# Optimization experiments

Hardware: AMD Instinct MI355X
Metric: run time of the kernel (lower is better)

The kernel has to match this reference:

```python
import jax, jax.numpy as jnp
import numpy as np

B, T, D = 4, 2048, 1024
H, DH, E, SEL = 8, 64, 5, 2


def setup_inputs() -> dict:
    key = jax.random.key(0)
    ks = jax.random.split(key, 7)
    s = 0.02
    x = jax.random.normal(ks[0], (B, T, D), dtype=jnp.float32)
    Wq = jax.random.normal(ks[1], (D, H * DH), dtype=jnp.float32) * s
    Wk = jax.random.normal(ks[2], (D, H * DH), dtype=jnp.float32) * s
    Ws = jax.random.normal(ks[3], (D, H * E), dtype=jnp.float32) * s   # gate for V experts
    Wd = jax.random.normal(ks[4], (D, H * E), dtype=jnp.float32) * s   # gate for out experts
    Wv = jax.random.normal(ks[5], (E, D, DH), dtype=jnp.float32) * s   # experts_v weights
    Wo = jax.random.normal(ks[6], (E, DH, D), dtype=jnp.float32) * s   # experts_out weights
    return {"x": x, "Wq": Wq, "Wk": Wk, "Ws": Ws, "Wd": Wd, "Wv": Wv, "Wo": Wo}


def _topk_mask(logits, k):
    # 0/1 mask of top-k experts along last axis (torch.topk indices are distinct)
    _, idx = jax.lax.top_k(logits, k)
    return jnp.sum(jax.nn.one_hot(idx, logits.shape[-1], dtype=logits.dtype), axis=-2)


def reference(x, Wq, Wk, Ws, Wd, Wv, Wo):
    e, d, dh = Wv.shape
    h = Wq.shape[1] // dh
    b, t, _ = x.shape
    scale = dh ** -0.5

    q = (x @ Wq).reshape(b, t, h, dh).transpose(0, 2, 1, 3)  # b h t d
    k = (x @ Wk).reshape(b, t, h, dh).transpose(0, 2, 1, 3)  # b h t d

    # moe_v: per-(b,t,head) top-k experts, sigmoid-weighted combine of expert V projections
    gl_v = (x @ Ws).reshape(b, t, h, e)                      # b t h e
    wv = _topk_mask(gl_v, SEL) * jax.nn.sigmoid(gl_v)        # b t h e (zero off selected)
    xv = jnp.einsum('btd,edk->btek', x, Wv)                  # all-expert V: b t e dh
    v = jnp.einsum('bthe,btek->bhtk', wv, xv)                # b h t dh

    scores = jnp.einsum('bhid,bhjd->bhij', q * scale, k)     # b h t t
    probs = jax.nn.softmax(scores, axis=-1)
    attn = jnp.einsum('bhij,bhjd->bihd', probs, v)           # b t h dh

    # moe_out: top-k selection (weights computed but unused in original), unweighted sum,
    # then sum over heads — fuse both reductions into one einsum
    gl_o = (x @ Wd).reshape(b, t, h, e)
    mask_o = _topk_mask(gl_o, SEL)                           # b t h e
    out = jnp.einsum('bthe,bthk,ekd->btd', mask_o, attn, Wo)  # b t d
    return out
```

## Files before the change

### kernel.cpp

```cpp
#include <hip/hip_runtime.h>
#include <cstdint>
#include <cstddef>

#define BB 4
#define TT 2048
#define DD 1024
#define HH 8
#define DH 64
#define EE 5
#define MM (BB*TT)
#define PLD 1344
#define NWT 1408

typedef short short8 __attribute__((ext_vector_type(8)));
typedef float f32x4  __attribute__((ext_vector_type(4)));
typedef float f32x16 __attribute__((ext_vector_type(16)));
typedef unsigned int u32x2 __attribute__((ext_vector_type(2)));

__device__ __forceinline__ float bflo(uint32_t u) { union { uint32_t i; float f; } v; v.i = u << 16; return v.f; }
__device__ __forceinline__ float bfhi(uint32_t u) { union { uint32_t i; float f; } v; v.i = u & 0xFFFF0000u; return v.f; }
__device__ __forceinline__ float bf2f(uint16_t u) { union { uint32_t i; float f; } v; v.i = ((uint32_t)u) << 16; return v.f; }
__device__ __forceinline__ uint32_t pkbf(float a, float b) {
  uint32_t ua = __float_as_uint(a) + 0x8000u;
  uint32_t ub = __float_as_uint(b) + 0x8000u;
  return __builtin_amdgcn_perm(ub, ua, 0x07060302u);
}
__device__ __forceinline__ uint16_t bfr1(float f) {
  return (uint16_t)((__float_as_uint(f) + 0x8000u) >> 16);
}
__device__ __forceinline__ uint32_t cvtpk(float a, float b) {
  uint32_t r;
  asm("v_cvt_pk_bf16_f32 %0, %1, %2" : "=v"(r) : "v"(a), "v"(b));
  return r;
}

__device__ __forceinline__ void gload16(const void* g, void* l) {
  __builtin_amdgcn_global_load_lds(
      (const __attribute__((address_space(1))) uint32_t*)g,
      (__attribute__((address_space(3))) uint32_t*)l, 16, 0, 0);
}

__global__ __launch_bounds__(256) void pack_wt_kernel(
    const float* __restrict__ Wq, const float* __restrict__ Wk,
    const float* __restrict__ Wv, uint16_t* __restrict__ Wt)
{
  __shared__ __align__(16) uint16_t Ts[64 * 68];
  int k0 = blockIdx.x * 64, n0 = blockIdx.y * 64;
  int t = threadIdx.x;
#pragma unroll
  for (int rep = 0; rep < 16; ++rep) {
    int li = rep * 256 + t;
    int kl = li >> 6, nl = li & 63;
    int k = k0 + kl, n = n0 + nl;
    float v = 0.f;
    if (n < 512)       v = Wq[k * 512 + n];
    else if (n < 1024) v = Wk[k * 512 + (n - 512)];
    else if (n < 1344) { int nn = n - 1024; v = Wv[((size_t)(nn >> 6) * 1024 + k) * 64 + (nn & 63)]; }
    Ts[kl * 68 + nl] = bfr1(v);
  }
  __syncthreads();
#pragma unroll
  for (int rep = 0; rep < 16; ++rep) {
    int li = rep * 256 + t;
    int nl = li >> 6, kl = li & 63;
    Wt[(size_t)(n0 + nl) * 1024 + k0 + kl] = Ts[kl * 68 + nl];
  }
}

__global__ __launch_bounds__(256) void pack_wot_kernel(
    const float* __restrict__ Wo, uint16_t* __restrict__ WoT)
{
  __shared__ __align__(16) uint16_t Ts[64 * 68];
  int k0 = blockIdx.x * 64, n0 = blockIdx.y * 64;
  int t = threadIdx.x;
#pragma unroll
  for (int rep = 0; rep < 16; ++rep) {
    int li = rep * 256 + t;
    int kl = li >> 6, nl = li & 63;
    Ts[kl * 68 + nl] = bfr1(Wo[(size_t)(k0 + kl) * 1024 + n0 + nl]);
  }
  __syncthreads();
#pragma unroll
  for (int rep = 0; rep < 16; ++rep) {
    int li = rep * 256 + t;
    int nl = li >> 6, kl = li & 63;
    WoT[(size_t)(n0 + nl) * 320 + k0 + kl] = Ts[kl * 68 + nl];
  }
}

__global__ __launch_bounds__(256) void xbf_kernel(const float* __restrict__ x, uint16_t* __restrict__ xb)
{
  int i = (blockIdx.x * 256 + threadIdx.x) * 4;
  float4 v = *(const float4*)(x + i);
  uint2 o;
  o.x = pkbf(v.x, v.y);
  o.y = pkbf(v.z, v.w);
  *(uint2*)(xb + i) = o;
}

__device__ __forceinline__ void top2_5(float g0, float g1, float g2, float g3, float g4,
                                       int& i1, float& b1, int& i2, float& b2) {
  i1 = 0; b1 = g0;
  if (g1 > b1) { b1 = g1; i1 = 1; }
  if (g2 > b1) { b1 = g2; i1 = 2; }
  if (g3 > b1) { b1 = g3; i1 = 3; }
  if (g4 > b1) { b1 = g4; i1 = 4; }
  i2 = -1; b2 = -__builtin_inff();
  if (i1 != 0 && g0 > b2) { b2 = g0; i2 = 0; }
  if (i1 != 1 && g1 > b2) { b2 = g1; i2 = 1; }
  if (i1 != 2 && g2 > b2) { b2 = g2; i2 = 2; }
  if (i1 != 3 && g3 > b2) { b2 = g3; i2 = 3; }
  if (i1 != 4 && g4 > b2) { b2 = g4; i2 = 4; }
}

__device__ __forceinline__ void ldw20(float* d, const float* __restrict__ p) {
#pragma unroll
  for (int j = 0; j < 20; ++j) d[j] = p[j];
}
__device__ __forceinline__ void fma20(float* acc, const float* wv, float xv) {
#pragma unroll
  for (int j = 0; j < 20; ++j) acc[j] = fmaf(xv, wv[j], acc[j]);
}

__global__ __launch_bounds__(1024) void gate_v6_kernel(
    const float* __restrict__ x, const float* __restrict__ Ws,
    const float* __restrict__ Wd, uint32_t* __restrict__ gsel32)
{
  __shared__ __align__(16) float xs[10752];
  int t = threadIdx.x;
  int m0 = blockIdx.x * 64;
  int g  = blockIdx.y;
  int w = t >> 6, lane = t & 63;
  int cg = __builtin_amdgcn_readfirstlane(w & 1);
  int kq = __builtin_amdgcn_readfirstlane(w >> 1);
  const float* __restrict__ Wg = g ? Wd : Ws;
  const float* __restrict__ wbase = Wg + (size_t)(kq * 16) * 40 + cg * 20;

  float acc[20];
#pragma unroll
  for (int j = 0; j < 20; ++j) acc[j] = 0.f;

  for (int tile = 0; tile < 8; ++tile) {
    __syncthreads();
#pragma unroll
    for (int rep = 0; rep < 2; ++rep) {
      int li = rep * 1024 + t;
      int row = li >> 5, kg = li & 31;
      float4 v = *(const float4*)&x[(size_t)(m0 + row) * 1024 + tile * 128 + kg * 4];
      *(float4*)&xs[row * 132 + kg * 4] = v;
    }
    __syncthreads();

    const float* wp = wbase + (size_t)tile * 128 * 40;
    const float* xp = &xs[lane * 132 + kq * 16];
    float wc[20], wn[20];
    ldw20(wc, wp);
#pragma unroll
    for (int k4 = 0; k4 < 4; ++k4) {
      float4 xv = *(const float4*)&xp[k4 * 4];
      ldw20(wn, wp + (size_t)(k4 * 4 + 1) * 40);
      fma20(acc, wc, xv.x);
      ldw20(wc, wp + (size_t)(k4 * 4 + 2) * 40);
      fma20(acc, wn, xv.y);
      ldw20(wn, wp + (size_t)(k4 * 4 + 3) * 40);
      fma20(acc, wc, xv.z);
      if (k4 < 3) ldw20(wc, wp + (size_t)(k4 * 4 + 4) * 40);
      fma20(acc, wn, xv.w);
    }
  }

  float* red = xs;
  __syncthreads();
  if (kq & 1) {
    int ro = (((kq >> 1) * 2 + cg) * 64 + lane) * 21;
#pragma unroll
    for (int j = 0; j < 20; ++j) red[ro + j] = acc[j];
  }
  __syncthreads();
  if (!(kq & 1)) {
    int ro = (((kq >> 1) * 2 + cg) * 64 + lane) * 21;
#pragma unroll
    for (int j = 0; j < 20; ++j) acc[j] += red[ro + j];
  }
  __syncthreads();
  if (kq == 2 || kq == 6) {
    int ro = (((kq >> 2) * 2 + cg) * 64 + lane) * 21;
#pragma unroll
    for (int j = 0; j < 20; ++j) red[ro + j] = acc[j];
  }
  __syncthreads();
  if (kq == 0 || kq == 4) {
    int ro = (((kq >> 2) * 2 + cg) * 64 + lane) * 21;
#pragma unroll
    for (int j = 0; j < 20; ++j) acc[j] += red[ro + j];
  }
  __syncthreads();
  if (kq == 4) {
    int ro = (cg * 64 + lane) * 21;
#pragma unroll
    for (int j = 0; j < 20; ++j) red[ro + j] = acc[j];
  }
  __syncthreads();

  if (kq == 0) {
    int ro = (cg * 64 + lane) * 21;
#pragma unroll
    for (int j = 0; j < 20; ++j) acc[j] += red[ro + j];
    int m = m0 + lane;
    if (g == 0) {
#pragma unroll
      for (int hh = 0; hh < 4; ++hh) {
        int i1, i2; float b1, b2;
        top2_5(acc[hh * 5 + 0], acc[hh * 5 + 1], acc[hh * 5 + 2],
               acc[hh * 5 + 3], acc[hh * 5 + 4], i1, b1, i2, b2);
        float w1 = 1.f / (1.f + __expf(-b1));
        float w2 = 1.f / (1.f + __expf(-b2));
        uint32_t* gp = gsel32 + ((size_t)m * 8 + cg * 4 + hh) * 4;
        gp[0] = __float_as_uint(w1);
        gp[1] = __float_as_uint(w2);
        gp[2] = (uint32_t)(i1 | (i2 << 3));
      }
    } else {
#pragma unroll
      for (int hh = 0; hh < 4; ++hh) {
        int j1, j2; float c1, c2;
        top2_5(acc[hh * 5 + 0], acc[hh * 5 + 1], acc[hh * 5 + 2],
               acc[hh * 5 + 3], acc[hh * 5 + 4], j1, c1, j2, c2);
        uint32_t* gp = gsel32 + ((size_t)m * 8 + cg * 4 + hh) * 4;
        gp[3] = (uint32_t)(j1 | (j2 << 3));
      }
    }
  }
}

__global__ __launch_bounds__(256) void proj_mfma_kernel(
    const uint16_t* __restrict__ xb, const uint16_t* __restrict__ Wt,
    uint16_t* __restrict__ proj)
{
  __shared__ __align__(16) uint16_t As[128 * 32];
  __shared__ __align__(16) uint16_t Bs[128 * 32];
  int t = threadIdx.x;
  int n0 = blockIdx.x * 128, m0 = blockIdx.y * 128;
  int w = t >> 6, lane = t & 63, q = lane >> 4, c = lane & 15;
  int wm = w & 1, wn = w >> 1;
  int lr = lane >> 2, lc = (lane & 3) * 8;
  f32x4 zf = {0.f, 0.f, 0.f, 0.f};
  f32x4 acc[4][4];
#pragma unroll
  for (int i = 0; i < 4; ++i)
#pragma unroll
    for (int j = 0; j < 4; ++j) acc[i][j] = zf;

  for (int kb = 0; kb < 32; ++kb) {
    __syncthreads();
#pragma unroll
    for (int j = 0; j < 2; ++j) {
      int row = w * 32 + j * 16 + lr;
      gload16(xb + (size_t)(m0 + row) * 1024 + kb * 32 + lc,
              &As[(w * 32 + j * 16) * 32 + lane * 8]);
      gload16(Wt + (size_t)(n0 + row) * 1024 + kb * 32 + lc,
              &Bs[(w * 32 + j * 16) * 32 + lane * 8]);
    }
    __syncthreads();
    short8 af[4], bfr[4];
#pragma unroll
    for (int i = 0; i < 4; ++i)
      af[i] = *(const short8*)&As[(wm * 64 + i * 16 + c) * 32 + q * 8];
#pragma unroll
    for (int j = 0; j < 4; ++j)
      bfr[j] = *(const short8*)&Bs[(wn * 64 + j * 16 + c) * 32 + q * 8];
#pragma unroll
    for (int i = 0; i < 4; ++i)
#pragma unroll
      for (int j = 0; j < 4; ++j)
        acc[i][j] = __builtin_amdgcn_mfma_f32_16x16x32_bf16(af[i], bfr[j], acc[i][j], 0, 0, 0);
  }
#pragma unroll
  for (int i = 0; i < 4; ++i)
#pragma unroll
    for (int j = 0; j < 4; ++j) {
      int col = n0 + wn * 64 + j * 16 + c;
      if (col < PLD) {
#pragma unroll
        for (int reg = 0; reg < 4; ++reg) {
          int row = m0 + wm * 64 + i * 16 + q * 4 + reg;
          proj[(size_t)row * PLD + col] = bfr1(acc[i][j][reg]);
        }
      }
    }
}

__global__ __launch_bounds__(256) void out_mfma_kernel(
    const uint16_t* __restrict__ zb, const uint16_t* __restrict__ WoT,
    float* __restrict__ out)
{
  __shared__ __align__(16) uint16_t As[128 * 32];
  __shared__ __align__(16) uint16_t Bs[128 * 32];
  int t = threadIdx.x;
  int n0 = blockIdx.x * 128, m0 = blockIdx.y * 128;
  int w = t >> 6, lane = t & 63, q = lane >> 4, c = lane & 15;
  int wm = w & 1, wn = w >> 1;
  int lr = lane >> 2, lc = (lane & 3) * 8;
  f32x4 zf = {0.f, 0.f, 0.f, 0.f};
  f32x4 acc[4][4];
#pragma unroll
  for (int i = 0; i < 4; ++i)
#pragma unroll
    for (int j = 0; j < 4; ++j) acc[i][j] = zf;

  for (int kb = 0; kb < 10; ++kb) {
    __syncthreads();
#pragma unroll
    for (int j = 0; j < 2; ++j) {
      int row = w * 32 + j * 16 + lr;
      gload16(zb + (size_t)(m0 + row) * 320 + kb * 32 + lc,
              &As[(w * 32 + j * 16) * 32 + lane * 8]);
      gload16(WoT + (size_t)(n0 + row) * 320 + kb * 32 + lc,
              &Bs[(w * 32 + j * 16) * 32 + lane * 8]);
    }
    __syncthreads();
    short8 af[4], bfr[4];
#pragma unroll
    for (int i = 0; i < 4; ++i)
      af[i] = *(const short8*)&As[(wm * 64 + i * 16 + c) * 32 + q * 8];
#pragma unroll
    for (int j = 0; j < 4; ++j)
      bfr[j] = *(const short8*)&Bs[(wn * 64 + j * 16 + c) * 32 + q * 8];
#pragma unroll
    for (int i = 0; i < 4; ++i)
#pragma unroll
      for (int j = 0; j < 4; ++j)
        acc[i][j] = __builtin_amdgcn_mfma_f32_16x16x32_bf16(af[i], bfr[j], acc[i][j], 0, 0, 0);
  }
#pragma unroll
  for (int i = 0; i < 4; ++i)
#pragma unroll
    for (int j = 0; j < 4; ++j) {
      int col = n0 + wn * 64 + j * 16 + c;
#pragma unroll
      for (int reg = 0; reg < 4; ++reg) {
        int row = m0 + wm * 64 + i * 16 + q * 4 + reg;
        out[(size_t)row * 1024 + col] = acc[i][j][reg];
      }
    }
}

__global__ __launch_bounds__(256) void vbuild_kernel(
    const uint16_t* __restrict__ proj, const uint4* __restrict__ gsel,
    uint16_t* __restrict__ vt)
{
  int bi = blockIdx.x;
  int bh = bi >> 5, tb = bi & 31;
  int b = bh >> 3, h = bh & 7;
  int t = threadIdx.x;
  int tt = t & 63, dg = t >> 6;
  int m = b * 2048 + tb * 64 + tt;
  uint4 gs = gsel[m * 8 + h];
  float w1 = __uint_as_float(gs.x), w2 = __uint_as_float(gs.y);
  int i1 = gs.z & 7, i2 = (gs.z >> 3) & 7;
  const uint16_t* base = proj + (size_t)m * PLD + 1024;
  const uint4* p1 = (const uint4*)(base + i1 * 64 + dg * 16);
  const uint4* p2 = (const uint4*)(base + i2 * 64 + dg * 16);
  uint4 A0 = p1[0], A1 = p1[1], B0 = p2[0], B1 = p2[1];
  float v[16];
  v[0]  = w1*bflo(A0.x) + w2*bflo(B0.x); v[1]  = w1*bfhi(A0.x) + w2*bfhi(B0.x);
  v[2]  = w1*bflo(A0.y) + w2*bflo(B0.y); v[3]  = w1*bfhi(A0.y) + w2*bfhi(B0.y);
  v[4]  = w1*bflo(A0.z) + w2*bflo(B0.z); v[5]  = w1*bfhi(A0.z) + w2*bfhi(B0.z);
  v[6]  = w1*bflo(A0.w) + w2*bflo(B0.w); v[7]  = w1*bfhi(A0.w) + w2*bfhi(B0.w);
  v[8]  = w1*bflo(A1.x) + w2*bflo(B1.x); v[9]  = w1*bfhi(A1.x) + w2*bfhi(B1.x);
  v[10] = w1*bflo(A1.y) + w2*bflo(B1.y); v[11] = w1*bfhi(A1.y) + w2*bfhi(B1.y);
  v[12] = w1*bflo(A1.z) + w2*bflo(B1.z); v[13] = w1*bfhi(A1.z) + w2*bfhi(B1.z);
  v[14] = w1*bflo(A1.w) + w2*bflo(B1.w); v[15] = w1*bfhi(A1.w) + w2*bfhi(B1.w);
#pragma unroll
  for (int dd = 0; dd < 16; ++dd)
    vt[(size_t)(bh * 64 + dg * 16 + dd) * 2048 + tb * 64 + tt] = bfr1(v[dd]);
}

__global__ __launch_bounds__(512) void flash_mfma_kernel(
    const uint16_t* __restrict__ proj, const uint16_t* __restrict__ vt,
    uint16_t* __restrict__ attnb)
{
  __shared__ __align__(16) char smem[36864];
  int t = threadIdx.x;
  int bx = blockIdx.x;
  int qb = bx & 15, bh = bx >> 4;
  int h = bh & 7, b = bh >> 3;
  int g = t >> 8;
  int tg = t & 255;
  int w = t >> 6, wl = w & 3;
  int lane = t & 63;
  int r31 = lane & 31, hi = lane >> 5;
  int srow = tg >> 2, scq = tg & 3;

  uint16_t* Ksg = (uint16_t*)smem + g * 4608;
  uint16_t* Vsg = (uint16_t*)smem + 9216 + g * 4608;

  short8 qf[4];
  {
    const uint16_t* qp = proj + (size_t)(b * 2048 + qb * 128 + wl * 32 + r31) * PLD + h * 64 + hi * 8;
#pragma unroll
    for (int f = 0; f < 4; ++f) qf[f] = *(const short8*)(qp + 16 * f);
  }

  f32x16 o0 = {0.f}, o1 = {0.f};
#pragma unroll
  for (int i = 0; i < 16; ++i) { o0[i] = 0.f; o1[i] = 0.f; }
  float lsacc = 0.f;

  const uint16_t* kg = proj + (size_t)(b * 2048 + g * 1024 + srow) * PLD + 512 + h * 64 + scq * 16;
  const uint16_t* vg = vt + (size_t)(bh * 64 + srow) * 2048 + g * 1024 + scq * 16;
  uint4 kp0, kp1, vp0, vp1;
  kp0 = ((const uint4*)kg)[0]; kp1 = ((const uint4*)kg)[1];
  vp0 = ((const uint4*)vg)[0]; vp1 = ((const uint4*)vg)[1];

  for (int it = 0; it < 16; ++it) {
    if (it) __syncthreads();
    *(uint4*)&Ksg[srow * 72 + scq * 16] = kp0;
    *(uint4*)&Ksg[srow * 72 + scq * 16 + 8] = kp1;
    *(uint4*)&Vsg[srow * 72 + scq * 16] = vp0;
    *(uint4*)&Vsg[srow * 72 + scq * 16 + 8] = vp1;
    __syncthreads();
    if (it < 15) {
      const uint4* pk = (const uint4*)(kg + (size_t)(it + 1) * 64 * PLD);
      kp0 = pk[0]; kp1 = pk[1];
      const uint4* pv = (const uint4*)(vg + (it + 1) * 64);
      vp0 = pv[0]; vp1 = pv[1];
    }

    short8 pa[4];
#pragma unroll
    for (int jg = 0; jg < 2; ++jg) {
      f32x16 s;
#pragma unroll
      for (int i = 0; i < 16; ++i) s[i] = 0.f;
#pragma unroll
      for (int f = 0; f < 4; ++f) {
        short8 kf = *(const short8*)&Ksg[(jg * 32 + r31) * 72 + hi * 8 + 16 * f];
        s = __builtin_amdgcn_mfma_f32_32x32x16_bf16(kf, qf[f], s, 0, 0, 0);
      }
      float p[16];
#pragma unroll
      for (int reg = 0; reg < 16; ++reg)
        p[reg] = __builtin_amdgcn_exp2f(s[reg] * 0.18033688f);
      lsacc += (((p[0] + p[1]) + (p[2] + p[3])) + ((p[4] + p[5]) + (p[6] + p[7])))
             + (((p[8] + p[9]) + (p[10] + p[11])) + ((p[12] + p[13]) + (p[14] + p[15])));
      uint32_t X1 = cvtpk(p[0], p[1]),  X2 = cvtpk(p[2], p[3]);
      uint32_t Y1 = cvtpk(p[4], p[5]),  Y2 = cvtpk(p[6], p[7]);
      uint32_t Z1 = cvtpk(p[8], p[9]),  Z2 = cvtpk(p[10], p[11]);
      uint32_t W1 = cvtpk(p[12], p[13]), W2 = cvtpk(p[14], p[15]);
      u32x2 s1 = __builtin_amdgcn_permlane32_swap(X1, Y1, false, false);
      u32x2 s2 = __builtin_amdgcn_permlane32_swap(X2, Y2, false, false);
      u32x2 s3 = __builtin_amdgcn_permlane32_swap(Z1, W1, false, false);
      u32x2 s4 = __builtin_amdgcn_permlane32_swap(Z2, W2, false, false);
      uint4 f0 = { s1.x, s2.x, s1.y, s2.y };
      uint4 f1 = { s3.x, s4.x, s3.y, s4.y };
      pa[jg * 2 + 0] = *(short8*)&f0;
      pa[jg * 2 + 1] = *(short8*)&f1;
    }

#pragma unroll
    for (int f = 0; f < 4; ++f) {
      short8 vf0 = *(const short8*)&Vsg[(r31) * 72 + hi * 8 + 16 * f];
      short8 vf1 = *(const short8*)&Vsg[(32 + r31) * 72 + hi * 8 + 16 * f];
      o0 = __builtin_amdgcn_mfma_f32_32x32x16_bf16(pa[f], vf0, o0, 0, 0, 0);
      o1 = __builtin_amdgcn_mfma_f32_32x32x16_bf16(pa[f], vf1, o1, 0, 0, 0);
    }
  }

  float lsc = lsacc + __shfl_xor(lsacc, 32);
  __syncthreads();
  float* xch = (float*)smem;
  float* xls = (float*)(smem + 33792);
  float* lsb = (float*)(smem + 34304);
  if (g == 1) {
    int base = (wl * 64 + lane) * 33;
#pragma unroll
    for (int reg = 0; reg < 16; ++reg) {
      xch[base + reg] = o0[reg];
      xch[base + 16 + reg] = o1[reg];
    }
    if (lane < 32) xls[wl * 32 + r31] = lsc;
  }
  __syncthreads();
  if (g == 0) {
    int base = (wl * 64 + lane) * 33;
#pragma unroll
    for (int reg = 0; reg < 16; ++reg) {
      o0[reg] += xch[base + reg];
      o1[reg] += xch[base + 16 + reg];
    }
    float lst = lsc + xls[wl * 32 + r31];
    if (lane < 32) lsb[wl * 32 + r31] = 1.0f / lst;
#pragma unroll
    for (int reg = 0; reg < 16; ++reg) {
      int r = (reg & 3) + 8 * (reg >> 2) + 4 * hi;
      float inv = lsb[wl * 32 + r];
      size_t row = (size_t)(b * 2048 + qb * 128 + wl * 32 + r);
      attnb[row * 512 + h * 64 + r31]      = bfr1(o0[reg] * inv);
      attnb[row * 512 + h * 64 + 32 + r31] = bfr1(o1[reg] * inv);
    }
  }
}

__global__ __launch_bounds__(64) void zbuild_kernel(
    const uint16_t* __restrict__ attnb, const uint32_t* __restrict__ gselw,
    uint16_t* __restrict__ zbuf)
{
  int m = blockIdx.x; int c = threadIdx.x;
  float acc[5] = {0.f, 0.f, 0.f, 0.f, 0.f};
#pragma unroll
  for (int h = 0; h < 8; ++h) {
    uint32_t sel = gselw[(m * 8 + h) * 4 + 3];
    int e1 = sel & 7, e2 = (sel >> 3) & 7;
    float a = bf2f(attnb[(size_t)m * 512 + h * 64 + c]);
#pragma unroll
    for (int e = 0; e < 5; ++e)
      acc[e] += (e == e1 || e == e2) ? a : 0.f;
  }
#pragma unroll
  for (int e = 0; e < 5; ++e)
    zbuf[(size_t)m * 320 + e * 64 + c] = bfr1(acc[e]);
}

extern "C" void kernel_launch(void* const* d_in, const int* in_sizes, int n_in,
                              void* d_out, int out_size, void* d_ws, size_t ws_size,
                              hipStream_t stream) {
  const float* x  = (const float*)d_in[0];
  const float* Wq = (const float*)d_in[1];
  const float* Wk = (const float*)d_in[2];
  const float* Ws = (const float*)d_in[3];
  const float* Wd = (const float*)d_in[4];
  const float* Wv = (const float*)d_in[5];
  const float* Wo = (const float*)d_in[6];
  float* out = (float*)d_out;

  char* ws = (char*)d_ws;
  uint4*    gsel  = (uint4*)   (ws);
  uint16_t* WoT   = (uint16_t*)(ws + 1048576);
  uint16_t* Wt    = (uint16_t*)(ws + 1703936);
  uint16_t* xb    = (uint16_t*)(ws + 4587520);
  uint16_t* proj  = (uint16_t*)(ws + 21364736);
  uint16_t* vt    = (uint16_t*)(ws + 43384832);
  uint16_t* attnb = (uint16_t*)(ws + 1703936);
  uint16_t* zbuf  = (uint16_t*)(ws + 10092544);

  gate_v6_kernel<<<dim3(MM / 64, 2), 1024, 0, stream>>>(x, Ws, Wd, (uint32_t*)gsel);
  pack_wt_kernel<<<dim3(16, 22), 256, 0, stream>>>(Wq, Wk, Wv, Wt);
  pack_wot_kernel<<<dim3(5, 16), 256, 0, stream>>>(Wo, WoT);
  xbf_kernel<<<(MM * DD / 4) / 256, 256, 0, stream>>>(x, xb);
  proj_mfma_kernel<<<dim3(NWT / 128, MM / 128), 256, 0, stream>>>(xb, Wt, proj);
  vbuild_kernel<<<32 * 32, 256, 0, stream>>>(proj, gsel, vt);
  flash_mfma_kernel<<<BB * HH * (TT / 128), 512, 0, stream>>>(proj, vt, attnb);
  zbuild_kernel<<<MM, 64, 0, stream>>>(attnb, (const uint32_t*)gsel, zbuf);
  out_mfma_kernel<<<dim3(DD / 128, MM / 128), 256, 0, stream>>>(zbuf, WoT, out);
}
```

Measured before the change: 236.5 us.

## Fuse x bf16 cast into gate kernel and double-buffer flash K/V tiles

The gate kernel now writes the bf16 copy of x while it stages x into shared memory, so the separate xbf_kernel launch and its second full read of x go away. The flash attention kernel switches to two K/V shared-memory buffers and processes tiles in pairs. This removes one barrier per tile and lets the stores for the next tile proceed while the current tile is computed. Shared memory per block doubles to 72KB, which may lower occupancy.

```diff
diff --git a/kernel.cpp b/kernel.cpp
--- a/kernel.cpp
+++ b/kernel.cpp
@@ -86,16 +86,6 @@
     int nl = li >> 6, kl = li & 63;
     WoT[(size_t)(n0 + nl) * 320 + k0 + kl] = Ts[kl * 68 + nl];
   }
-}
-
-__global__ __launch_bounds__(256) void xbf_kernel(const float* __restrict__ x, uint16_t* __restrict__ xb)
-{
-  int i = (blockIdx.x * 256 + threadIdx.x) * 4;
-  float4 v = *(const float4*)(x + i);
-  uint2 o;
-  o.x = pkbf(v.x, v.y);
-  o.y = pkbf(v.z, v.w);
-  *(uint2*)(xb + i) = o;
 }
 
 __device__ __forceinline__ void top2_5(float g0, float g1, float g2, float g3, float g4,
@@ -122,9 +112,10 @@
   for (int j = 0; j < 20; ++j) acc[j] = fmaf(xv, wv[j], acc[j]);
 }
 
-__global__ __launch_bounds__(1024) void gate_v6_kernel(
+__global__ __launch_bounds__(1024) void gate_v7_kernel(
     const float* __restrict__ x, const float* __restrict__ Ws,
-    const float* __restrict__ Wd, uint32_t* __restrict__ gsel32)
+    const float* __restrict__ Wd, uint32_t* __restrict__ gsel32,
+    uint16_t* __restrict__ xb)
 {
   __shared__ __align__(16) float xs[10752];
   int t = threadIdx.x;
@@ -146,8 +137,15 @@
     for (int rep = 0; rep < 2; ++rep) {
       int li = rep * 1024 + t;
       int row = li >> 5, kg = li & 31;
-      float4 v = *(const float4*)&x[(size_t)(m0 + row) * 1024 + tile * 128 + kg * 4];
+      size_t off = (size_t)(m0 + row) * 1024 + tile * 128 + kg * 4;
+      float4 v = *(const float4*)&x[off];
       *(float4*)&xs[row * 132 + kg * 4] = v;
+      if (g == 0) {
+        uint2 o;
+        o.x = pkbf(v.x, v.y);
+        o.y = pkbf(v.z, v.w);
+        *(uint2*)&xb[off] = o;
+      }
     }
     __syncthreads();
 
@@ -376,11 +374,55 @@
     vt[(size_t)(bh * 64 + dg * 16 + dd) * 2048 + tb * 64 + tt] = bfr1(v[dd]);
 }
 
+__device__ __forceinline__ void flash_step(
+    const uint16_t* Ksg, const uint16_t* Vsg,
+    const short8 (&qf)[4], f32x16& o0, f32x16& o1, float& lsacc,
+    int r31, int hi)
+{
+  short8 pa[4];
+#pragma unroll
+  for (int jg = 0; jg < 2; ++jg) {
+    f32x16 s;
+#pragma unroll
+    for (int i = 0; i < 16; ++i) s[i] = 0.f;
+#pragma unroll
+    for (int f = 0; f < 4; ++f) {
+      short8 kf = *(const short8*)&Ksg[(jg * 32 + r31) * 72 + hi * 8 + 16 * f];
+      s = __builtin_amdgcn_mfma_f32_32x32x16_bf16(kf, qf[f], s, 0, 0, 0);
+    }
+    float p[16];
+#pragma unroll
+    for (int reg = 0; reg < 16; ++reg)
+      p[reg] = __builtin_amdgcn_exp2f(s[reg] * 0.18033688f);
+    lsacc += (((p[0] + p[1]) + (p[2] + p[3])) + ((p[4] + p[5]) + (p[6] + p[7])))
+           + (((p[8] + p[9]) + (p[10] + p[11])) + ((p[12] + p[13]) + (p[14] + p[15])));
+    uint32_t X1 = cvtpk(p[0], p[1]),  X2 = cvtpk(p[2], p[3]);
+    uint32_t Y1 = cvtpk(p[4], p[5]),  Y2 = cvtpk(p[6], p[7]);
+    uint32_t Z1 = cvtpk(p[8], p[9]),  Z2 = cvtpk(p[10], p[11]);
+    uint32_t W1 = cvtpk(p[12], p[13]), W2 = cvtpk(p[14], p[15]);
+    u32x2 s1 = __builtin_amdgcn_permlane32_swap(X1, Y1, false, false);
+    u32x2 s2 = __builtin_amdgcn_permlane32_swap(X2, Y2, false, false);
+    u32x2 s3 = __builtin_amdgcn_permlane32_swap(Z1, W1, false, false);
+    u32x2 s4 = __builtin_amdgcn_permlane32_swap(Z2, W2, false, false);
+    uint4 f0 = { s1.x, s2.x, s1.y, s2.y };
+    uint4 f1 = { s3.x, s4.x, s3.y, s4.y };
+    pa[jg * 2 + 0] = *(short8*)&f0;
+    pa[jg * 2 + 1] = *(short8*)&f1;
+  }
+#pragma unroll
+  for (int f = 0; f < 4; ++f) {
+    short8 vf0 = *(const short8*)&Vsg[(r31) * 72 + hi * 8 + 16 * f];
+    short8 vf1 = *(const short8*)&Vsg[(32 + r31) * 72 + hi * 8 + 16 * f];
+    o0 = __builtin_amdgcn_mfma_f32_32x32x16_bf16(pa[f], vf0, o0, 0, 0, 0);
+    o1 = __builtin_amdgcn_mfma_f32_32x32x16_bf16(pa[f], vf1, o1, 0, 0, 0);
+  }
+}
+
 __global__ __launch_bounds__(512) void flash_mfma_kernel(
     const uint16_t* __restrict__ proj, const uint16_t* __restrict__ vt,
     uint16_t* __restrict__ attnb)
 {
-  __shared__ __align__(16) char smem[36864];
+  __shared__ __align__(16) char smem[73728];
   int t = threadIdx.x;
   int bx = blockIdx.x;
   int qb = bx & 15, bh = bx >> 4;
@@ -392,8 +434,11 @@
   int r31 = lane & 31, hi = lane >> 5;
   int srow = tg >> 2, scq = tg & 3;
 
-  uint16_t* Ksg = (uint16_t*)smem + g * 4608;
-  uint16_t* Vsg = (uint16_t*)smem + 9216 + g * 4608;
+  uint16_t* K0 = (uint16_t*)(smem)         + g * 4608;
+  uint16_t* V0 = (uint16_t*)(smem + 18432) + g * 4608;
+  uint16_t* K1 = (uint16_t*)(smem + 36864) + g * 4608;
+  uint16_t* V1 = (uint16_t*)(smem + 55296) + g * 4608;
+  int so = srow * 72 + scq * 16;
 
   short8 qf[4];
   {
@@ -409,66 +454,44 @@
 
   const uint16_t* kg = proj + (size_t)(b * 2048 + g * 1024 + srow) * PLD + 512 + h * 64 + scq * 16;
   const uint16_t* vg = vt + (size_t)(bh * 64 + srow) * 2048 + g * 1024 + scq * 16;
+
   uint4 kp0, kp1, vp0, vp1;
   kp0 = ((const uint4*)kg)[0]; kp1 = ((const uint4*)kg)[1];
   vp0 = ((const uint4*)vg)[0]; vp1 = ((const uint4*)vg)[1];
-
-  for (int it = 0; it < 16; ++it) {
-    if (it) __syncthreads();
-    *(uint4*)&Ksg[srow * 72 + scq * 16] = kp0;
-    *(uint4*)&Ksg[srow * 72 + scq * 16 + 8] = kp1;
-    *(uint4*)&Vsg[srow * 72 + scq * 16] = vp0;
-    *(uint4*)&Vsg[srow * 72 + scq * 16 + 8] = vp1;
-    __syncthreads();
-    if (it < 15) {
-      const uint4* pk = (const uint4*)(kg + (size_t)(it + 1) * 64 * PLD);
+  *(uint4*)&K0[so] = kp0; *(uint4*)&K0[so + 8] = kp1;
+  *(uint4*)&V0[so] = vp0; *(uint4*)&V0[so + 8] = vp1;
+  {
+    const uint4* pk = (const uint4*)(kg + (size_t)64 * PLD);
+    kp0 = pk[0]; kp1 = pk[1];
+    const uint4* pv = (const uint4*)(vg + 64);
+    vp0 = pv[0]; vp1 = pv[1];
+  }
+  __syncthreads();
+
+  for (int it2 = 0; it2 < 8; ++it2) {
+    *(uint4*)&K1[so] = kp0; *(uint4*)&K1[so + 8] = kp1;
+    *(uint4*)&V1[so] = vp0; *(uint4*)&V1[so + 8] = vp1;
+    if (it2 < 7) {
+      const uint4* pk = (const uint4*)(kg + (size_t)(2 * it2 + 2) * 64 * PLD);
       kp0 = pk[0]; kp1 = pk[1];
-      const uint4* pv = (const uint4*)(vg + (it + 1) * 64);
+      const uint4* pv = (const uint4*)(vg + (2 * it2 + 2) * 64);
       vp0 = pv[0]; vp1 = pv[1];
     }
-
-    short8 pa[4];
-#pragma unroll
-    for (int jg = 0; jg < 2; ++jg) {
-      f32x16 s;
-#pragma unroll
-      for (int i = 0; i < 16; ++i) s[i] = 0.f;
-#pragma unroll
-      for (int f = 0; f < 4; ++f) {
-        short8 kf = *(const short8*)&Ksg[(jg * 32 + r31) * 72 + hi * 8 + 16 * f];
-        s = __builtin_amdgcn_mfma_f32_32x32x16_bf16(kf, qf[f], s, 0, 0, 0);
-      }
-      float p[16];
-#pragma unroll
-      for (int reg = 0; reg < 16; ++reg)
-        p[reg] = __builtin_amdgcn_exp2f(s[reg] * 0.18033688f);
-      lsacc += (((p[0] + p[1]) + (p[2] + p[3])) + ((p[4] + p[5]) + (p[6] + p[7])))
-             + (((p[8] + p[9]) + (p[10] + p[11])) + ((p[12] + p[13]) + (p[14] + p[15])));
-      uint32_t X1 = cvtpk(p[0], p[1]),  X2 = cvtpk(p[2], p[3]);
-      uint32_t Y1 = cvtpk(p[4], p[5]),  Y2 = cvtpk(p[6], p[7]);
-      uint32_t Z1 = cvtpk(p[8], p[9]),  Z2 = cvtpk(p[10], p[11]);
-      uint32_t W1 = cvtpk(p[12], p[13]), W2 = cvtpk(p[14], p[15]);
-      u32x2 s1 = __builtin_amdgcn_permlane32_swap(X1, Y1, false, false);
-      u32x2 s2 = __builtin_amdgcn_permlane32_swap(X2, Y2, false, false);
-      u32x2 s3 = __builtin_amdgcn_permlane32_swap(Z1, W1, false, false);
-      u32x2 s4 = __builtin_amdgcn_permlane32_swap(Z2, W2, false, false);
-      uint4 f0 = { s1.x, s2.x, s1.y, s2.y };
-      uint4 f1 = { s3.x, s4.x, s3.y, s4.y };
-      pa[jg * 2 + 0] = *(short8*)&f0;
-      pa[jg * 2 + 1] = *(short8*)&f1;
-    }
-
-#pragma unroll
-    for (int f = 0; f < 4; ++f) {
-      short8 vf0 = *(const short8*)&Vsg[(r31) * 72 + hi * 8 + 16 * f];
-      short8 vf1 = *(const short8*)&Vsg[(32 + r31) * 72 + hi * 8 + 16 * f];
-      o0 = __builtin_amdgcn_mfma_f32_32x32x16_bf16(pa[f], vf0, o0, 0, 0, 0);
-      o1 = __builtin_amdgcn_mfma_f32_32x32x16_bf16(pa[f], vf1, o1, 0, 0, 0);
-    }
+    flash_step(K0, V0, qf, o0, o1, lsacc, r31, hi);
+    __syncthreads();
+    if (it2 < 7) {
+      *(uint4*)&K0[so] = kp0; *(uint4*)&K0[so + 8] = kp1;
+      *(uint4*)&V0[so] = vp0; *(uint4*)&V0[so + 8] = vp1;
+      const uint4* pk = (const uint4*)(kg + (size_t)(2 * it2 + 3) * 64 * PLD);
+      kp0 = pk[0]; kp1 = pk[1];
+      const uint4* pv = (const uint4*)(vg + (2 * it2 + 3) * 64);
+      vp0 = pv[0]; vp1 = pv[1];
+    }
+    flash_step(K1, V1, qf, o0, o1, lsacc, r31, hi);
+    __syncthreads();
   }
 
   float lsc = lsacc + __shfl_xor(lsacc, 32);
-  __syncthreads();
   float* xch = (float*)smem;
   float* xls = (float*)(smem + 33792);
   float* lsb = (float*)(smem + 34304);
@@ -544,10 +567,9 @@
   uint16_t* attnb = (uint16_t*)(ws + 1703936);
   uint16_t* zbuf  = (uint16_t*)(ws + 10092544);
 
-  gate_v6_kernel<<<dim3(MM / 64, 2), 1024, 0, stream>>>(x, Ws, Wd, (uint32_t*)gsel);
+  gate_v7_kernel<<<dim3(MM / 64, 2), 1024, 0, stream>>>(x, Ws, Wd, (uint32_t*)gsel, xb);
   pack_wt_kernel<<<dim3(16, 22), 256, 0, stream>>>(Wq, Wk, Wv, Wt);
   pack_wot_kernel<<<dim3(5, 16), 256, 0, stream>>>(Wo, WoT);
-  xbf_kernel<<<(MM * DD / 4) / 256, 256, 0, stream>>>(x, xb);
   proj_mfma_kernel<<<dim3(NWT / 128, MM / 128), 256, 0, stream>>>(xb, Wt, proj);
   vbuild_kernel<<<32 * 32, 256, 0, stream>>>(proj, gsel, vt);
   flash_mfma_kernel<<<BB * HH * (TT / 128), 512, 0, stream>>>(proj, vt, attnb);
```

Result: faster. 230.4 us (-2.6%).
